# Kernel optimization log

Hardware: AMD Instinct MI355X
Metric: run time of the kernel (lower is better)

The kernel has to match this reference:

```python
import jax, jax.numpy as jnp
import numpy as np

DIM = 512
HEADS = 16
WS = 7  # window size (cube), N = WS**3 = 343
B_ = 128
N = WS ** 3
TABLE = (2 * WS - 1) ** 3  # 2197


def _relative_position_index():
    coords = np.stack(np.meshgrid(np.arange(WS), np.arange(WS), np.arange(WS), indexing='ij'))  # [3,WS,WS,WS]
    cf = coords.reshape(3, -1)  # [3, N]
    rel = cf[:, :, None] - cf[:, None, :]  # [3, N, N]
    rel = rel.transpose(1, 2, 0).copy()
    rel[:, :, 0] += WS - 1
    rel[:, :, 1] += WS - 1
    rel[:, :, 2] += WS - 1
    rel[:, :, 0] *= (2 * WS - 1) * (2 * WS - 1)
    rel[:, :, 1] *= 2 * WS - 1
    return jnp.asarray(rel.sum(-1), dtype=jnp.int32)  # [N, N]


def setup_inputs() -> dict:
    key = jax.random.key(0)
    ks = jax.random.split(key, 8)
    x = jax.random.normal(ks[0], (B_, N, DIM), dtype=jnp.float32)
    q_global = jax.random.normal(ks[1], (1, DIM), dtype=jnp.float32)
    qkv_w = jax.random.normal(ks[2], (3 * DIM, DIM), dtype=jnp.float32) * (DIM ** -0.5)
    qkv_b = jax.random.normal(ks[3], (3 * DIM,), dtype=jnp.float32) * 0.02
    proj_w = jax.random.normal(ks[4], (DIM, DIM), dtype=jnp.float32) * (DIM ** -0.5)
    proj_b = jax.random.normal(ks[5], (DIM,), dtype=jnp.float32) * 0.02
    rel_bias_table = jax.random.normal(ks[6], (TABLE, HEADS), dtype=jnp.float32) * 0.02
    rel_pos_index = _relative_position_index()
    return {"x": x, "q_global": q_global, "qkv_w": qkv_w, "qkv_b": qkv_b,
            "rel_bias_table": rel_bias_table, "proj_w": proj_w, "proj_b": proj_b,
            "rel_pos_index": rel_pos_index}


def reference(x, q_global, qkv_w, qkv_b, rel_bias_table, proj_w, proj_b, rel_pos_index):
    B, Nt, C = x.shape
    hd = C // HEADS
    scale = hd ** -0.5
    # QKV projection (torch Linear: x @ W.T + b)
    qkv = (x @ qkv_w.T + qkv_b).reshape(B, Nt, 3, HEADS, hd)
    qkv = jnp.transpose(qkv, (2, 0, 3, 1, 4))  # [3, B, H, N, hd]
    q, k, v = qkv[0] * scale, qkv[1], qkv[2]
    attn = jnp.einsum('bhqd,bhkd->bhqk', q, k)  # [B, H, N, N]
    # relative position bias gather: table[idx] -> [N, N, H] -> [H, N, N]
    bias = rel_bias_table[rel_pos_index.reshape(-1)].reshape(Nt, Nt, HEADS)
    attn = attn + jnp.transpose(bias, (2, 0, 1))[None]
    attn = jax.nn.softmax(attn, axis=-1)
    out = jnp.einsum('bhqk,bhkd->bhqd', attn, v)  # [B, H, N, hd]
    out = jnp.transpose(out, (0, 2, 1, 3)).reshape(B, Nt, C)
    return out @ proj_w.T + proj_b
```

## Files before the change

### kernel.cpp

```cpp
#include <hip/hip_runtime.h>

typedef unsigned short u16;
typedef __attribute__((ext_vector_type(8))) short short8;
typedef __attribute__((ext_vector_type(4))) float f32x4;
typedef __attribute__((ext_vector_type(16))) float f32x16;
typedef __attribute__((ext_vector_type(4))) unsigned uint4v;

#define NTOK 343
#define DIMC 512
#define HEADS_ 16
#define BATCH 128
#define MROWS 43904
#define TBL 117649

#define LOG2E 1.4426950408889634f
#define QSCALE (0.17677669529663687f * LOG2E)

__device__ __forceinline__ u16 f2bf(float f) {
  unsigned u = __builtin_bit_cast(unsigned, f);
  unsigned r = (u + 0x7fffu + ((u >> 16) & 1u)) >> 16;
  return (u16)r;
}
__device__ __forceinline__ float bf2f(u16 x) {
  return __builtin_bit_cast(float, ((unsigned)x) << 16);
}
__device__ __forceinline__ unsigned cvtpk(float lo, float hi) {
  unsigned r;
  asm("v_cvt_pk_bf16_f32 %0, %1, %2" : "=v"(r) : "v"(lo), "v"(hi));
  return r;
}

__global__ void cvt_f32_bf16_k(const float* __restrict__ in, u16* __restrict__ out, int n4) {
  int i = blockIdx.x * blockDim.x + threadIdx.x;
  int st = gridDim.x * blockDim.x;
  for (; i < n4; i += st) {
    float4 v = reinterpret_cast<const float4*>(in)[i];
    ushort4 o;
    o.x = f2bf(v.x); o.y = f2bf(v.y); o.z = f2bf(v.z); o.w = f2bf(v.w);
    reinterpret_cast<ushort4*>(out)[i] = o;
  }
}

__global__ void bias_pre_k(const float* __restrict__ table, const int* __restrict__ idx,
                           u16* __restrict__ biasB) {
  int t = blockIdx.x * 256 + threadIdx.x;
  if (t >= HEADS_ * 121 * 256) return;
  int r4 = t & 3;
  int l = (t >> 2) & 63;
  int rest = t >> 8;
  int tq = rest % 11;
  int nt = (rest / 11) % 11;
  int h = rest / 121;
  int q = tq * 32 + (l & 31);
  int hi = l >> 5;
  ushort4 o;
  u16* oe = (u16*)&o;
#pragma unroll
  for (int rr = 0; rr < 4; ++rr) {
    int r = r4 * 4 + rr;
    int tok = nt * 32 + (r & 3) + 8 * (r >> 2) + 4 * hi;
    float v = (q < NTOK && tok < NTOK) ? (LOG2E * table[idx[q * NTOK + tok] * HEADS_ + h])
                                       : -1e30f;
    oe[rr] = f2bf(v);
  }
  *reinterpret_cast<ushort4*>(biasB +
                              (size_t)(((h * 11 + nt) * 11 + tq) * 1024 + l * 16 + r4 * 4)) = o;
}

#define GLD16(gptr, lptr)                                                        \
  __builtin_amdgcn_global_load_lds(                                              \
      (const __attribute__((address_space(1))) void*)(const void*)(gptr),        \
      (__attribute__((address_space(3))) void*)(void*)(lptr), 16, 0, 0)

template <int EPI>
__global__ __launch_bounds__(256) void gemm_bt_k(const u16* __restrict__ A,
                                                 const u16* __restrict__ B,
                                                 const float* __restrict__ bias,
                                                 void* __restrict__ C, int N, int K) {
  const int NBL = N >> 7;
  int nwg = gridDim.x;
  int orig = blockIdx.x;
  int qq = nwg >> 3, rr = nwg & 7;
  int xcd = orig & 7, lid = orig >> 3;
  int bid = (xcd < rr ? xcd * (qq + 1) : rr * (qq + 1) + (xcd - rr) * qq) + lid;
  int mb = bid / NBL, nb = bid % NBL;
  __shared__ __align__(16) u16 As[2][128 * 32];
  __shared__ __align__(16) u16 Bs[2][128 * 32];
  int tid = threadIdx.x;
  int w = tid >> 6, l = tid & 63;
  int wr = w >> 1, wc = w & 1;
  f32x4 acc[4][4];
#pragma unroll
  for (int i = 0; i < 4; i++)
#pragma unroll
    for (int j = 0; j < 4; j++) acc[i][j] = (f32x4){0.f, 0.f, 0.f, 0.f};

  const int srow_in = l >> 2;
  const int scb = l & 3;

#define STG2(kt, slot)                                                                    \
  {                                                                                       \
    _Pragma("unroll") for (int i4 = 0; i4 < 2; ++i4) {                                    \
      int rowl = w * 32 + i4 * 16 + srow_in;                                              \
      int cbs = (scb * 16) ^ (((rowl >> 1) & 3) << 4);     \
      GLD16(A + (size_t)(mb * 128 + rowl) * K + (kt)*32 + (cbs >> 1),                     \
            As[slot] + (w * 32 + i4 * 16) * 32 + l * 8);                                  \
      GLD16(B + (size_t)(nb * 128 + rowl) * K + (kt)*32 + (cbs >> 1),                     \
            Bs[slot] + (w * 32 + i4 * 16) * 32 + l * 8);                                  \
    }                                                                                     \
  }

  int KT = K >> 5;
  STG2(0, 0);
  __syncthreads();
  for (int kt = 0; kt < KT; ++kt) {
    int cur = kt & 1;
    if (kt + 1 < KT) STG2(kt + 1, cur ^ 1);
    {
      short8 af[4], bf[4];
#pragma unroll
      for (int i = 0; i < 4; i++) {
        int row = wr * 64 + i * 16 + (l & 15);
        int off = row * 64 + (((l >> 4) * 16) ^ (((row >> 1) & 3) << 4));
        af[i] = *reinterpret_cast<const short8*>((const u16*)As[cur] + (off >> 1));
      }
#pragma unroll
      for (int j = 0; j < 4; j++) {
        int row = wc * 64 + j * 16 + (l & 15);
        int off = row * 64 + (((l >> 4) * 16) ^ (((row >> 1) & 3) << 4));
        bf[j] = *reinterpret_cast<const short8*>((const u16*)Bs[cur] + (off >> 1));
      }
#pragma unroll
      for (int i = 0; i < 4; i++)
#pragma unroll
        for (int j = 0; j < 4; j++)
          acc[i][j] = __builtin_amdgcn_mfma_f32_16x16x32_bf16(af[i], bf[j], acc[i][j], 0, 0, 0);
    }
    __syncthreads();
  }
#undef STG2

  int r0 = mb * 128 + wr * 64 + (l >> 4) * 4;
  int c0 = nb * 128 + wc * 64 + (l & 15);
#pragma unroll
  for (int j = 0; j < 4; j++) {
    int col = c0 + j * 16;
    float bv = bias[col];
    float mul = (EPI == 0 && col < 512) ? QSCALE : 1.0f;
#pragma unroll
    for (int i = 0; i < 4; i++) {
      int row = r0 + i * 16;
      if (EPI == 0) {
        u16* Cp = (u16*)C + (size_t)row * N + col;
#pragma unroll
        for (int r = 0; r < 4; r += 2) {
          unsigned pk = cvtpk((acc[i][j][r] + bv) * mul, (acc[i][j][r + 1] + bv) * mul);
          Cp[(size_t)r * N] = (u16)pk;
          Cp[(size_t)(r + 1) * N] = (u16)(pk >> 16);
        }
      } else {
#pragma unroll
        for (int r = 0; r < 4; r++)
          ((float*)C)[(size_t)(row + r) * N + col] = acc[i][j][r] + bv;
      }
    }
  }
}

__global__ __launch_bounds__(256, 3) void attn_k(const u16* __restrict__ qkv,
                                                 const u16* __restrict__ biasB,
                                                 u16* __restrict__ outA) {
  int p = blockIdx.x;
  int jj = p >> 3;
  int h = 2 * (p & 7) + (jj >> 7);
  int b = jj & 127;
  __shared__ __align__(16) u16 kS[352 * 40];
  __shared__ __align__(16) u16 vT[32 * 370];
  int tid = threadIdx.x;

  for (int idx = tid; idx < 352 * 4; idx += 256) {
    int row = idx >> 2, seg = idx & 3;
    uint4 vk = {0, 0, 0, 0};
    if (row < NTOK)
      vk = *reinterpret_cast<const uint4*>(qkv + (size_t)(b * NTOK + row) * 1536 + 512 +
                                           h * 32 + seg * 8);
    *reinterpret_cast<uint4*>(kS + row * 40 + seg * 8) = vk;
  }
  for (int idx = tid; idx < NTOK * 4; idx += 256) {
    int row = idx >> 2, seg = idx & 3;
    size_t base = (size_t)(b * NTOK + row) * 1536 + 1024 + h * 32 + seg * 8;
    uint4 vv = *reinterpret_cast<const uint4*>(qkv + base);
    const u16* e = reinterpret_cast<const u16*>(&vv);
#pragma unroll
    for (int t = 0; t < 8; ++t) vT[(seg * 8 + t) * 370 + row] = e[t];
  }
  for (int idx = tid; idx < 32 * 9; idx += 256) vT[(idx / 9) * 370 + NTOK + (idx % 9)] = 0;
  __syncthreads();

  int w = tid >> 6, l = tid & 63;
  const int d32 = l & 31, hi = l >> 5;
  const bool upHalf = (hi != 0);

  for (int tq = w; tq < 11; tq += 4) {
    int qrow = tq * 32 + d32;
    short8 bq0 = (short8){0, 0, 0, 0, 0, 0, 0, 0};
    short8 bq1 = (short8){0, 0, 0, 0, 0, 0, 0, 0};
    if (qrow < NTOK) {
      const u16* qb = qkv + (size_t)(b * NTOK + qrow) * 1536 + h * 32 + hi * 8;
      bq0 = *reinterpret_cast<const short8*>(qb);
      bq1 = *reinterpret_cast<const short8*>(qb + 16);
    }
    f32x16 O = {0, 0, 0, 0, 0, 0, 0, 0, 0, 0, 0, 0, 0, 0, 0, 0};
    float tot = 0.f;
    const u16* bbase = biasB + ((size_t)(h * 121 + tq)) * 1024 + l * 16;
    for (int nt = 0; nt < 11; ++nt) {
      const u16* kr = kS + (nt * 32 + d32) * 40 + hi * 8;
      short8 ak0 = *reinterpret_cast<const short8*>(kr);
      short8 ak1 = *reinterpret_cast<const short8*>(kr + 16);
      f32x16 S = {0, 0, 0, 0, 0, 0, 0, 0, 0, 0, 0, 0, 0, 0, 0, 0};
      S = __builtin_amdgcn_mfma_f32_32x32x16_bf16(ak0, bq0, S, 0, 0, 0);
      S = __builtin_amdgcn_mfma_f32_32x32x16_bf16(ak1, bq1, S, 0, 0, 0);
      const u16* bp = bbase + (size_t)nt * 11 * 1024;
      short8 bb0 = *reinterpret_cast<const short8*>(bp);
      short8 bb1 = *reinterpret_cast<const short8*>(bp + 8);
      float ex[16];
#pragma unroll
      for (int r = 0; r < 16; ++r) {
        u16 bw = (u16)((r < 8) ? bb0[r] : bb1[r - 8]);
        float v = S[r] + bf2f(bw);
        ex[r] = __builtin_amdgcn_exp2f(v);
        tot += ex[r];
      }
      unsigned W[8];
#pragma unroll
      for (int r2 = 0; r2 < 8; ++r2) W[r2] = cvtpk(ex[2 * r2], ex[2 * r2 + 1]);
#pragma unroll
      for (int c = 0; c < 2; ++c) {
        unsigned x0 = W[4 * c + 0], x1 = W[4 * c + 1];
        unsigned y0 = W[4 * c + 2], y1 = W[4 * c + 3];
        unsigned x0s = (unsigned)__shfl_xor((int)x0, 32);
        unsigned x1s = (unsigned)__shfl_xor((int)x1, 32);
        unsigned y0s = (unsigned)__shfl_xor((int)y0, 32);
        unsigned y1s = (unsigned)__shfl_xor((int)y1, 32);
        uint4v ap;
        ap.x = upHalf ? y0s : x0;
        ap.y = upHalf ? y1s : x1;
        ap.z = upHalf ? y0 : x0s;
        ap.w = upHalf ? y1 : x1s;
        short8 bv = *reinterpret_cast<const short8*>(vT + d32 * 370 + nt * 32 + c * 16 + hi * 8);
        O = __builtin_amdgcn_mfma_f32_32x32x16_bf16(__builtin_bit_cast(short8, ap), bv, O,
                                                    0, 0, 0);
      }
    }
    tot += __builtin_bit_cast(float, __shfl_xor(__builtin_bit_cast(int, tot), 32));
    float inv = 1.0f / tot;
#pragma unroll
    for (int r = 0; r < 16; ++r) {
      int qloc = (r & 3) + 8 * (r >> 2) + 4 * hi;
      float ir = __shfl(inv, qloc);
      int q = tq * 32 + qloc;
      if (q < NTOK) {
        float ov = O[r] * ir;
        outA[(size_t)(b * NTOK + q) * 512 + h * 32 + d32] = (u16)cvtpk(ov, ov);
      }
    }
  }
}

extern "C" void kernel_launch(void* const* d_in, const int* in_sizes, int n_in,
                              void* d_out, int out_size, void* d_ws, size_t ws_size,
                              hipStream_t stream) {
  const float* x      = (const float*)d_in[0];
  const float* qkv_w  = (const float*)d_in[2];
  const float* qkv_b  = (const float*)d_in[3];
  const float* table  = (const float*)d_in[4];
  const float* proj_w = (const float*)d_in[5];
  const float* proj_b = (const float*)d_in[6];
  const int*   relidx = (const int*)d_in[7];

  char* ws = (char*)d_ws;
  u16*   x_bf  = (u16*)(ws);
  u16*   qw_bf = (u16*)(ws + 44957696);
  u16*   pw_bf = (u16*)(ws + 46530560);
  u16*   qkv_o = (u16*)(ws + 47054848);
  u16*   biasB = (u16*)(ws + 181927936);

  cvt_f32_bf16_k<<<2048, 256, 0, stream>>>(x, x_bf, (BATCH * NTOK * DIMC) / 4);
  cvt_f32_bf16_k<<<768, 256, 0, stream>>>(qkv_w, qw_bf, (3 * DIMC * DIMC) / 4);
  cvt_f32_bf16_k<<<256, 256, 0, stream>>>(proj_w, pw_bf, (DIMC * DIMC) / 4);
  bias_pre_k<<<1936, 256, 0, stream>>>(table, relidx, biasB);

  gemm_bt_k<0><<<343 * 12, 256, 0, stream>>>(x_bf, qw_bf, qkv_b, qkv_o, 1536, 512);
  attn_k<<<BATCH * HEADS_, 256, 0, stream>>>(qkv_o, biasB, x_bf);
  gemm_bt_k<1><<<343 * 4, 256, 0, stream>>>(x_bf, pw_bf, proj_b, d_out, 512, 512);
}
```

Measured before the change: 266.9 us.

## Fuse x fp32-to-bf16 conversion into QKV GEMM loads and pack V transpose

The QKV GEMM now stages fp32 x tiles straight into LDS with a swizzled layout and converts them to bf16 while building the MFMA fragments. This removes the separate conversion kernel and its bf16 round trip of x through memory. In exchange the A tile in LDS doubles in size and conversion work moves into the inner loop. Separately, the attention kernel's V transpose now pairs adjacent rows with lane shuffles and writes 32-bit words into LDS instead of scattered 16-bit stores.

```diff
diff --git a/kernel.cpp b/kernel.cpp
--- a/kernel.cpp
+++ b/kernel.cpp
@@ -73,7 +73,7 @@
       (__attribute__((address_space(3))) void*)(void*)(lptr), 16, 0, 0)
 
 template <int EPI>
-__global__ __launch_bounds__(256) void gemm_bt_k(const u16* __restrict__ A,
+__global__ __launch_bounds__(256) void gemm_bt_k(const void* __restrict__ Av,
                                                  const u16* __restrict__ B,
                                                  const float* __restrict__ bias,
                                                  void* __restrict__ C, int N, int K) {
@@ -84,11 +84,14 @@
   int xcd = orig & 7, lid = orig >> 3;
   int bid = (xcd < rr ? xcd * (qq + 1) : rr * (qq + 1) + (xcd - rr) * qq) + lid;
   int mb = bid / NBL, nb = bid % NBL;
-  __shared__ __align__(16) u16 As[2][128 * 32];
+  __shared__ __align__(16) char AsRaw[EPI == 0 ? 32768 : 16384];
   __shared__ __align__(16) u16 Bs[2][128 * 32];
+  float* AsF = (float*)AsRaw;
+  u16* AsB = (u16*)AsRaw;
   int tid = threadIdx.x;
   int w = tid >> 6, l = tid & 63;
   int wr = w >> 1, wc = w & 1;
+  int cl = l & 15, q4 = l >> 4;
   f32x4 acc[4][4];
 #pragma unroll
   for (int i = 0; i < 4; i++)
@@ -98,16 +101,37 @@
   const int srow_in = l >> 2;
   const int scb = l & 3;
 
-#define STG2(kt, slot)                                                                    \
+#define STGA32(kt, slot)                                                                  \
+  {                                                                                       \
+    _Pragma("unroll") for (int i4 = 0; i4 < 4; ++i4) {                                    \
+      int rowl = w * 32 + i4 * 8 + (l >> 3);                                              \
+      int blk = (l & 7) ^ (rowl & 7);                      \
+      GLD16((const float*)Av + (size_t)(mb * 128 + rowl) * K + (kt)*32 + blk * 4,         \
+            AsF + (slot)*4096 + (w * 32 + i4 * 8) * 32 + l * 4);                          \
+    }                                                                                     \
+  }
+#define STGA16(kt, slot)                                                                  \
   {                                                                                       \
     _Pragma("unroll") for (int i4 = 0; i4 < 2; ++i4) {                                    \
       int rowl = w * 32 + i4 * 16 + srow_in;                                              \
-      int cbs = (scb * 16) ^ (((rowl >> 1) & 3) << 4);     \
-      GLD16(A + (size_t)(mb * 128 + rowl) * K + (kt)*32 + (cbs >> 1),                     \
-            As[slot] + (w * 32 + i4 * 16) * 32 + l * 8);                                  \
+      int cbs = (scb * 16) ^ (((rowl >> 1) & 3) << 4);                                    \
+      GLD16((const u16*)Av + (size_t)(mb * 128 + rowl) * K + (kt)*32 + (cbs >> 1),        \
+            AsB + (slot)*4096 + (w * 32 + i4 * 16) * 32 + l * 8);                         \
+    }                                                                                     \
+  }
+#define STGB(kt, slot)                                                                    \
+  {                                                                                       \
+    _Pragma("unroll") for (int i4 = 0; i4 < 2; ++i4) {                                    \
+      int rowl = w * 32 + i4 * 16 + srow_in;                                              \
+      int cbs = (scb * 16) ^ (((rowl >> 1) & 3) << 4);                                    \
       GLD16(B + (size_t)(nb * 128 + rowl) * K + (kt)*32 + (cbs >> 1),                     \
             Bs[slot] + (w * 32 + i4 * 16) * 32 + l * 8);                                  \
     }                                                                                     \
+  }
+#define STG2(kt, slot)                                 \
+  {                                                    \
+    if (EPI == 0) STGA32(kt, slot) else STGA16(kt, slot) \
+    STGB(kt, slot)                                     \
   }
 
   int KT = K >> 5;
@@ -120,14 +144,27 @@
       short8 af[4], bf[4];
 #pragma unroll
       for (int i = 0; i < 4; i++) {
-        int row = wr * 64 + i * 16 + (l & 15);
-        int off = row * 64 + (((l >> 4) * 16) ^ (((row >> 1) & 3) << 4));
-        af[i] = *reinterpret_cast<const short8*>((const u16*)As[cur] + (off >> 1));
+        int row = wr * 64 + i * 16 + cl;
+        if (EPI == 0) {
+          const float* Ap = AsF + cur * 4096 + row * 32;
+          int b0 = (2 * q4) ^ (row & 7), b1 = (2 * q4 + 1) ^ (row & 7);
+          float4 a0 = *reinterpret_cast<const float4*>(Ap + b0 * 4);
+          float4 a1 = *reinterpret_cast<const float4*>(Ap + b1 * 4);
+          uint4v ua;
+          ua.x = cvtpk(a0.x, a0.y);
+          ua.y = cvtpk(a0.z, a0.w);
+          ua.z = cvtpk(a1.x, a1.y);
+          ua.w = cvtpk(a1.z, a1.w);
+          af[i] = __builtin_bit_cast(short8, ua);
+        } else {
+          int off = row * 64 + ((q4 * 16) ^ (((row >> 1) & 3) << 4));
+          af[i] = *reinterpret_cast<const short8*>(AsB + cur * 4096 + (off >> 1));
+        }
       }
 #pragma unroll
       for (int j = 0; j < 4; j++) {
-        int row = wc * 64 + j * 16 + (l & 15);
-        int off = row * 64 + (((l >> 4) * 16) ^ (((row >> 1) & 3) << 4));
+        int row = wc * 64 + j * 16 + cl;
+        int off = row * 64 + ((q4 * 16) ^ (((row >> 1) & 3) << 4));
         bf[j] = *reinterpret_cast<const short8*>((const u16*)Bs[cur] + (off >> 1));
       }
 #pragma unroll
@@ -139,9 +176,12 @@
     __syncthreads();
   }
 #undef STG2
-
-  int r0 = mb * 128 + wr * 64 + (l >> 4) * 4;
-  int c0 = nb * 128 + wc * 64 + (l & 15);
+#undef STGA32
+#undef STGA16
+#undef STGB
+
+  int r0 = mb * 128 + wr * 64 + q4 * 4;
+  int c0 = nb * 128 + wc * 64 + cl;
 #pragma unroll
   for (int j = 0; j < 4; j++) {
     int col = c0 + j * 16;
@@ -186,15 +226,33 @@
                                            h * 32 + seg * 8);
     *reinterpret_cast<uint4*>(kS + row * 40 + seg * 8) = vk;
   }
-  for (int idx = tid; idx < NTOK * 4; idx += 256) {
+  for (int idx = tid; idx < 344 * 4; idx += 256) {
     int row = idx >> 2, seg = idx & 3;
-    size_t base = (size_t)(b * NTOK + row) * 1536 + 1024 + h * 32 + seg * 8;
-    uint4 vv = *reinterpret_cast<const uint4*>(qkv + base);
-    const u16* e = reinterpret_cast<const u16*>(&vv);
-#pragma unroll
-    for (int t = 0; t < 8; ++t) vT[(seg * 8 + t) * 370 + row] = e[t];
-  }
-  for (int idx = tid; idx < 32 * 9; idx += 256) vT[(idx / 9) * 370 + NTOK + (idx % 9)] = 0;
+    uint4 vv = {0, 0, 0, 0};
+    if (row < NTOK)
+      vv = *reinterpret_cast<const uint4*>(qkv + (size_t)(b * NTOK + row) * 1536 + 1024 +
+                                           h * 32 + seg * 8);
+    unsigned ox = (unsigned)__shfl_xor((int)vv.x, 4);
+    unsigned oy = (unsigned)__shfl_xor((int)vv.y, 4);
+    unsigned oz = (unsigned)__shfl_xor((int)vv.z, 4);
+    unsigned ow = (unsigned)__shfl_xor((int)vv.w, 4);
+    unsigned* vT32 = (unsigned*)vT;
+    int rp = row >> 1;
+    if ((row & 1) == 0) {
+      int d0 = seg * 8;
+      vT32[(d0 + 0) * 185 + rp] = (vv.x & 0xFFFFu) | (ox << 16);
+      vT32[(d0 + 1) * 185 + rp] = (vv.x >> 16) | (ox & 0xFFFF0000u);
+      vT32[(d0 + 2) * 185 + rp] = (vv.y & 0xFFFFu) | (oy << 16);
+      vT32[(d0 + 3) * 185 + rp] = (vv.y >> 16) | (oy & 0xFFFF0000u);
+    } else {
+      int d0 = seg * 8 + 4;
+      vT32[(d0 + 0) * 185 + rp] = (oz & 0xFFFFu) | (vv.z << 16);
+      vT32[(d0 + 1) * 185 + rp] = (oz >> 16) | (vv.z & 0xFFFF0000u);
+      vT32[(d0 + 2) * 185 + rp] = (ow & 0xFFFFu) | (vv.w << 16);
+      vT32[(d0 + 3) * 185 + rp] = (ow >> 16) | (vv.w & 0xFFFF0000u);
+    }
+  }
+  for (int idx = tid; idx < 32 * 8; idx += 256) vT[(idx / 8) * 370 + 344 + (idx % 8)] = 0;
   __syncthreads();
 
   int w = tid >> 6, l = tid & 63;
@@ -279,18 +337,17 @@
   const int*   relidx = (const int*)d_in[7];
 
   char* ws = (char*)d_ws;
-  u16*   x_bf  = (u16*)(ws);
+  u16*   attnO = (u16*)(ws);
   u16*   qw_bf = (u16*)(ws + 44957696);
   u16*   pw_bf = (u16*)(ws + 46530560);
   u16*   qkv_o = (u16*)(ws + 47054848);
   u16*   biasB = (u16*)(ws + 181927936);
 
-  cvt_f32_bf16_k<<<2048, 256, 0, stream>>>(x, x_bf, (BATCH * NTOK * DIMC) / 4);
   cvt_f32_bf16_k<<<768, 256, 0, stream>>>(qkv_w, qw_bf, (3 * DIMC * DIMC) / 4);
   cvt_f32_bf16_k<<<256, 256, 0, stream>>>(proj_w, pw_bf, (DIMC * DIMC) / 4);
   bias_pre_k<<<1936, 256, 0, stream>>>(table, relidx, biasB);
 
-  gemm_bt_k<0><<<343 * 12, 256, 0, stream>>>(x_bf, qw_bf, qkv_b, qkv_o, 1536, 512);
-  attn_k<<<BATCH * HEADS_, 256, 0, stream>>>(qkv_o, biasB, x_bf);
-  gemm_bt_k<1><<<343 * 4, 256, 0, stream>>>(x_bf, pw_bf, proj_b, d_out, 512, 512);
-}
+  gemm_bt_k<0><<<343 * 12, 256, 0, stream>>>(x, qw_bf, qkv_b, qkv_o, 1536, 512);
+  attn_k<<<BATCH * HEADS_, 256, 0, stream>>>(qkv_o, biasB, attnO);
+  gemm_bt_k<1><<<343 * 4, 256, 0, stream>>>(attnO, pw_bf, proj_b, d_out, 512, 512);
+}
```

Measured after the change: 302.8 us. +13.5%, slower.
